# Kernel optimization log

Hardware: AMD Instinct MI355X
Metric: run time of the kernel (lower is better)

Reference implementation:

```python
import jax, jax.numpy as jnp
import numpy as np

D_MODEL = 1024
D_STATE = 64
D_CONV = 4
EXPAND = 2
HEADDIM = 128
NGROUPS = 1
D_INNER = EXPAND * D_MODEL                      # 2048
NHEADS = D_INNER // HEADDIM                     # 16
CONV_DIM = D_INNER + 2 * NGROUPS * D_STATE      # 2176
D_IN_PROJ = 2 * D_INNER + 2 * NGROUPS * D_STATE + NHEADS  # 4240
CHUNK = 64
B, L = 4, 2048


def segsum(x):
    # x: (..., l) -> (..., l, l); entry [i, j] = sum_{k=j+1..i} x_k (lower-tri, -inf above)
    l = x.shape[-1]
    cs = jnp.cumsum(x, -1)
    d = cs[..., :, None] - cs[..., None, :]
    mask = jnp.tril(jnp.ones((l, l), bool))
    return jnp.where(mask, d, -jnp.inf)


def setup_inputs() -> dict:
    key = jax.random.key(0)
    ks = jax.random.split(key, 8)
    x = jax.random.normal(ks[0], (B, L), jnp.float32)
    w_embed = jax.random.normal(ks[1], (D_MODEL,), jnp.float32)       # Linear(1, d_model) weight
    ln_g = jnp.ones((D_MODEL,), jnp.float32)
    ln_b = jnp.zeros((D_MODEL,), jnp.float32)
    W_in = jax.random.normal(ks[2], (D_IN_PROJ, D_MODEL), jnp.float32) * 0.02
    conv_w = jax.random.normal(ks[3], (CONV_DIM, D_CONV), jnp.float32) * 0.1
    conv_b = jnp.zeros((CONV_DIM,), jnp.float32)
    dt0 = jnp.exp(jax.random.uniform(ks[4], (NHEADS,), jnp.float32) * (np.log(0.1) - np.log(0.001)) + np.log(0.001))
    dt_bias = jnp.log(jnp.expm1(dt0))  # inverse softplus (mamba2 init)
    A_log = jnp.log(jax.random.uniform(ks[5], (NHEADS,), jnp.float32, minval=1.0, maxval=16.0))
    D = jnp.ones((NHEADS,), jnp.float32)
    rms_w = jnp.ones((D_INNER,), jnp.float32)
    W_out = jax.random.normal(ks[6], (D_MODEL, D_INNER), jnp.float32) * 0.02
    return {"x": x, "w_embed": w_embed, "ln_g": ln_g, "ln_b": ln_b, "W_in": W_in,
            "conv_w": conv_w, "conv_b": conv_b, "dt_bias": dt_bias, "A_log": A_log,
            "D": D, "rms_w": rms_w, "W_out": W_out}


def reference(x, w_embed, ln_g, ln_b, W_in, conv_w, conv_b, dt_bias, A_log, D, rms_w, W_out):
    # in_proj: Linear(1, d_model, bias=False)
    h = x[..., None] * w_embed                     # (B, L, d_model)
    # LayerNorm
    mu = jnp.mean(h, -1, keepdims=True)
    var = jnp.mean((h - mu) ** 2, -1, keepdims=True)
    h = (h - mu) * jax.lax.rsqrt(var + 1e-5) * ln_g + ln_b
    # ---- Mamba2 block ----
    zxbcdt = h @ W_in.T                            # (B, L, D_IN_PROJ)
    z, xBC, dt = jnp.split(zxbcdt, [D_INNER, D_INNER + CONV_DIM], axis=-1)
    dt = jax.nn.softplus(dt + dt_bias)             # (B, L, H)
    # causal depthwise conv1d + silu
    xp = jnp.pad(xBC, ((0, 0), (D_CONV - 1, 0), (0, 0)))
    conv = conv_b + sum(xp[:, k:k + L, :] * conv_w[:, k] for k in range(D_CONV))
    xBC = jax.nn.silu(conv)
    xs, Bm, Cm = jnp.split(xBC, [D_INNER, D_INNER + NGROUPS * D_STATE], axis=-1)
    X = xs.reshape(B, L, NHEADS, HEADDIM)
    rep = NHEADS // NGROUPS
    Bh = jnp.repeat(Bm.reshape(B, L, NGROUPS, D_STATE), rep, axis=2)   # (B,L,H,N)
    Ch = jnp.repeat(Cm.reshape(B, L, NGROUPS, D_STATE), rep, axis=2)
    A = -jnp.exp(A_log)                            # (H,)
    dA = dt * A                                    # (B, L, H)
    Xd = X * dt[..., None]                         # (B, L, H, P)
    # chunked SSD scan (math-equivalent to the selective-scan recurrence)
    nc = L // CHUNK
    Xc = Xd.reshape(B, nc, CHUNK, NHEADS, HEADDIM)
    Bc = Bh.reshape(B, nc, CHUNK, NHEADS, D_STATE)
    Cc = Ch.reshape(B, nc, CHUNK, NHEADS, D_STATE)
    Ac = dA.reshape(B, nc, CHUNK, NHEADS).transpose(0, 3, 1, 2)        # (B,H,c,l)
    Acs = jnp.cumsum(Ac, -1)
    Lmat = jnp.exp(segsum(Ac))                                          # (B,H,c,l,l)
    Y_diag = jnp.einsum('bclhn,bcshn,bhcls,bcshp->bclhp', Cc, Bc, Lmat, Xc)
    decay_states = jnp.exp(Acs[..., -1:] - Acs)
    states = jnp.einsum('bclhn,bhcl,bclhp->bchpn', Bc, decay_states, Xc)
    states = jnp.concatenate([jnp.zeros_like(states[:, :1]), states], axis=1)
    decay_chunk = jnp.exp(segsum(jnp.pad(Acs[..., -1], ((0, 0), (0, 0), (1, 0)))))
    prev_states = jnp.einsum('bhzc,bchpn->bzhpn', decay_chunk, states)[:, :-1]
    Y_off = jnp.einsum('bclhn,bchpn,bhcl->bclhp', Cc, prev_states, jnp.exp(Acs))
    Y = (Y_diag + Y_off).reshape(B, L, NHEADS, HEADDIM) + X * D[None, None, :, None]
    y = Y.reshape(B, L, D_INNER)
    # gated RMSNorm then out_proj
    y = y * jax.nn.silu(z)
    y = y * jax.lax.rsqrt(jnp.mean(y * y, -1, keepdims=True) + 1e-5) * rms_w
    return y @ W_out.T
```

## Files before the change

kernel.cpp:

```cpp
#include <hip/hip_runtime.h>

#define DEV __device__ __forceinline__

typedef __bf16 bf16x8 __attribute__((ext_vector_type(8)));
typedef float f32x4 __attribute__((ext_vector_type(4)));

#define BB 4
#define LL 2048
#define DMODEL 1024
#define DINNER 2048
#define NHEADS 16
#define HEADDIM 128
#define DSTATE 64
#define CONVDIM 2176
#define DINPROJ 4240
#define NCHUNK 32
#define ROWS (BB*LL)

#define OF_A    ((size_t)0)
#define OF_ST   ((size_t)32768)
#define OF_P    ((size_t)65536)
#define OF_Q    ((size_t)98304)
#define OF_WO   ((size_t)131072)
#define OF_CONV ((size_t)8388608)
#define OF_Y    ((size_t)50331648)
#define OF_YBF  ((size_t)100663296)
#define OF_SP   ((size_t)150994944)
#define OF_ACS  ((size_t)190840832)
#define OF_ECS  ((size_t)191365120)

DEV void gload_lds16(const void* g, void* l) {
  __builtin_amdgcn_global_load_lds((const __attribute__((address_space(1))) void*)g,
                                   (__attribute__((address_space(3))) void*)l, 16, 0, 0);
}

DEV char* swaddr(char* base, int r, int c) {
  return base + r * 128 + (((c) * 2) ^ (((r) & 7) << 4));
}

__global__ __launch_bounds__(256) void stats_kernel(
    const float* __restrict__ w, float* __restrict__ st)
{
  int t = threadIdx.x;
  float s = 0.f, s2 = 0.f;
  #pragma unroll
  for (int j = 0; j < 4; j++) { float v = w[t + 256 * j]; s += v; s2 += v * v; }
  #pragma unroll
  for (int m = 32; m; m >>= 1) { s += __shfl_xor(s, m); s2 += __shfl_xor(s2, m); }
  __shared__ float rs[4], rs2[4];
  if ((t & 63) == 0) { rs[t >> 6] = s; rs2[t >> 6] = s2; }
  __syncthreads();
  if (t == 0) {
    float S = rs[0] + rs[1] + rs[2] + rs[3];
    float S2 = rs2[0] + rs2[1] + rs2[2] + rs2[3];
    float mu = S * (1.f / DMODEL);
    st[0] = mu;
    st[1] = S2 * (1.f / DMODEL) - mu * mu;
  }
}

__global__ __launch_bounds__(256) void prep_a_kernel(
    const float* __restrict__ x, const float* __restrict__ st, float* __restrict__ a)
{
  int r = blockIdx.x * 256 + threadIdx.x;
  float varw = st[1];
  float xv = x[r];
  a[r] = xv * rsqrtf(xv * xv * varw + 1e-5f);
}

__global__ __launch_bounds__(256) void gemv_kernel(
    const float* __restrict__ w, const float* __restrict__ g,
    const float* __restrict__ beta, const float* __restrict__ st,
    const float* __restrict__ W, float* __restrict__ p, float* __restrict__ q)
{
  int t = threadIdx.x;
  int j = blockIdx.x * 16 + (t >> 4);
  int l16 = t & 15;
  float wbar = st[0];
  const float* Wr = W + (size_t)j * DMODEL;
  float ap = 0.f, aq = 0.f;
  #pragma unroll 4
  for (int jj = 0; jj < 64; jj++) {
    int i = jj * 16 + l16;
    float Wv = Wr[i];
    ap += (w[i] - wbar) * g[i] * Wv;
    aq += beta[i] * Wv;
  }
  #pragma unroll
  for (int m = 8; m; m >>= 1) { ap += __shfl_xor(ap, m, 16); aq += __shfl_xor(aq, m, 16); }
  if (l16 == 0) { p[j] = ap; q[j] = aq; }
}

__global__ __launch_bounds__(256) void convert_wo_kernel(
    const float* __restrict__ Wo, __bf16* __restrict__ Wob)
{
  const int NO = DMODEL * DINNER;
  for (int i = blockIdx.x * 256 + threadIdx.x; i < NO; i += gridDim.x * 256)
    Wob[i] = (__bf16)Wo[i];
}

__global__ __launch_bounds__(256) void conv2_kernel(
    const float* __restrict__ a, const float* __restrict__ p,
    const float* __restrict__ q, const float* __restrict__ conv_w,
    const float* __restrict__ conv_b, __bf16* __restrict__ out)
{
  int gidx = blockIdx.x * 256 + threadIdx.x;
  if (gidx >= ROWS * (CONVDIM / 8)) return;
  int cg = gidx % (CONVDIM / 8);
  int row = gidx / (CONVDIM / 8);
  int l = row & (LL - 1);
  int ch = cg * 8;
  float av[4];
  #pragma unroll
  for (int k = 0; k < 4; k++) {
    int li = l + k - 3;
    av[k] = (li >= 0) ? a[row + k - 3] : 0.f;
  }
  bf16x8 o;
  #pragma unroll
  for (int jj = 0; jj < 8; jj++) {
    int c = ch + jj;
    f32x4 cw = *(const f32x4*)(conv_w + c * 4);
    float px = p[DINNER + c], qx = q[DINNER + c];
    float sacw = 0.f, scw = 0.f;
    #pragma unroll
    for (int k = 0; k < 4; k++) {
      int li = l + k - 3;
      if (li >= 0) { sacw += av[k] * cw[k]; scw += cw[k]; }
    }
    float val = conv_b[c] + qx * scw + px * sacw;
    o[jj] = (__bf16)(val / (1.f + __expf(-val)));
  }
  *(bf16x8*)(out + (size_t)row * CONVDIM + ch) = o;
}

__global__ __launch_bounds__(256) void ssd_chunk_kernel(
    const __bf16* __restrict__ conv, const float* __restrict__ a,
    const float* __restrict__ p, const float* __restrict__ q,
    const float* __restrict__ dt_bias, const float* __restrict__ A_log,
    __bf16* __restrict__ Y, __bf16* __restrict__ S,
    float* __restrict__ acs, float* __restrict__ ecs)
{
  __shared__ __align__(16) char sm[49664];
  char* smC  = sm;
  char* smB  = sm + 8192;
  char* smBd = sm + 16384;
  char* smG  = sm + 24576;
  char* smX  = sm + 32768;
  float* sAcs = (float*)(sm + 49152);
  float* sDec = (float*)(sm + 49408);

  int bx = blockIdx.x;
  int c = bx & 31, h = (bx >> 5) & 15, b = bx >> 9;
  int t = threadIdx.x;
  int lane = t & 63, w = t >> 6;
  int row0 = b * LL + c * 64;
  const __bf16* cr = conv + (size_t)(row0 + lane) * CONVDIM;

  float av = a[row0 + lane];
  float vx = av * p[DINNER + CONVDIM + h] + q[DINNER + CONVDIM + h] + dt_bias[h];
  float dtv = vx > 15.f ? vx : log1pf(__expf(vx));

  bf16x8 bch[2], cch[2], xch[4];
  #pragma unroll
  for (int k = 0; k < 2; k++) {
    int c8 = w * 16 + 8 * k;
    bch[k] = *(const bf16x8*)(cr + DINNER + c8);
    cch[k] = *(const bf16x8*)(cr + DINNER + DSTATE + c8);
  }
  #pragma unroll
  for (int k = 0; k < 4; k++)
    xch[k] = *(const bf16x8*)(cr + h * HEADDIM + w * 8 + 32 * k);

  if (t < 64) {
    float Ah = -__expf(A_log[h]);
    float cs = dtv * Ah;
    #pragma unroll
    for (int off = 1; off < 64; off <<= 1) {
      float o = __shfl_up(cs, off);
      if (lane >= off) cs += o;
    }
    float cend = __shfl(cs, 63);
    sAcs[lane] = cs;
    sDec[lane] = __expf(cend - cs);
    acs[(((size_t)b * NHEADS + h) * NCHUNK + c) * 64 + lane] = cs;
    if (lane == 63) ecs[((size_t)b * NHEADS + h) * NCHUNK + c] = __expf(cend);
  }

  #pragma unroll
  for (int k = 0; k < 2; k++) {
    int c8 = w * 16 + 8 * k;
    *(bf16x8*)swaddr(smB, lane, c8) = bch[k];
    *(bf16x8*)swaddr(smC, lane, c8) = cch[k];
  }
  #pragma unroll
  for (int k = 0; k < 4; k++) {
    int p0 = w * 8 + 32 * k;
    #pragma unroll
    for (int j = 0; j < 8; j++)
      *(__bf16*)swaddr(smX, p0 + j, lane) = (__bf16)((float)xch[k][j] * dtv);
  }
  __syncthreads();

  float decv = sDec[lane];
  #pragma unroll
  for (int k = 0; k < 2; k++) {
    int c8 = w * 16 + 8 * k;
    #pragma unroll
    for (int j = 0; j < 8; j++)
      *(__bf16*)swaddr(smBd, c8 + j, lane) = (__bf16)((float)bch[k][j] * decv);
  }

  int lr = lane & 15, kb = (lane >> 4) * 8;
  int rl = 16 * w + (lane >> 4) * 4;

  {
    bf16x8 af[2];
    #pragma unroll
    for (int ks = 0; ks < 2; ks++)
      af[ks] = *(const bf16x8*)swaddr(smC, 16 * w + lr, ks * 32 + kb);
    f32x4 g[4] = {};
    #pragma unroll
    for (int nt = 0; nt < 4; nt++)
      #pragma unroll
      for (int ks = 0; ks < 2; ks++) {
        bf16x8 bm = *(const bf16x8*)swaddr(smB, 16 * nt + lr, ks * 32 + kb);
        g[nt] = __builtin_amdgcn_mfma_f32_16x16x32_bf16(af[ks], bm, g[nt], 0, 0, 0);
      }
    #pragma unroll
    for (int nt = 0; nt < 4; nt++)
      #pragma unroll
      for (int qq = 0; qq < 4; qq++) {
        int gl = rl + qq, gs = 16 * nt + lr;
        float val = (gl >= gs) ? g[nt][qq] * __expf(sAcs[gl] - sAcs[gs]) : 0.f;
        *(__bf16*)swaddr(smG, gl, gs) = (__bf16)val;
      }
  }
  __syncthreads();

  {
    bf16x8 af[2];
    #pragma unroll
    for (int ks = 0; ks < 2; ks++)
      af[ks] = *(const bf16x8*)swaddr(smG, 16 * w + lr, ks * 32 + kb);
    f32x4 y[8] = {};
    #pragma unroll
    for (int nt = 0; nt < 8; nt++)
      #pragma unroll
      for (int ks = 0; ks < 2; ks++) {
        bf16x8 bm = *(const bf16x8*)swaddr(smX, 16 * nt + lr, ks * 32 + kb);
        y[nt] = __builtin_amdgcn_mfma_f32_16x16x32_bf16(af[ks], bm, y[nt], 0, 0, 0);
      }
    #pragma unroll
    for (int nt = 0; nt < 8; nt++)
      #pragma unroll
      for (int qq = 0; qq < 4; qq++)
        Y[(size_t)(row0 + rl + qq) * DINNER + h * HEADDIM + 16 * nt + lr] = (__bf16)y[nt][qq];
  }

  {
    bf16x8 bfs[4][2];
    #pragma unroll
    for (int nt = 0; nt < 4; nt++)
      #pragma unroll
      for (int ks = 0; ks < 2; ks++)
        bfs[nt][ks] = *(const bf16x8*)swaddr(smBd, 16 * nt + lr, ks * 32 + kb);
    f32x4 s4[2][4] = {};
    #pragma unroll
    for (int mi = 0; mi < 2; mi++) {
      bf16x8 af[2];
      #pragma unroll
      for (int ks = 0; ks < 2; ks++)
        af[ks] = *(const bf16x8*)swaddr(smX, 32 * w + 16 * mi + lr, ks * 32 + kb);
      #pragma unroll
      for (int nt = 0; nt < 4; nt++)
        #pragma unroll
        for (int ks = 0; ks < 2; ks++)
          s4[mi][nt] = __builtin_amdgcn_mfma_f32_16x16x32_bf16(af[ks], bfs[nt][ks], s4[mi][nt], 0, 0, 0);
    }
    __bf16* Sp = S + (((size_t)b * NCHUNK + c) * NHEADS + h) * (HEADDIM * DSTATE);
    #pragma unroll
    for (int mi = 0; mi < 2; mi++)
      #pragma unroll
      for (int nt = 0; nt < 4; nt++)
        #pragma unroll
        for (int qq = 0; qq < 4; qq++) {
          int pp = 32 * w + 16 * mi + (lane >> 4) * 4 + qq;
          Sp[pp * DSTATE + 16 * nt + lr] = (__bf16)s4[mi][nt][qq];
        }
  }
}

__global__ __launch_bounds__(256) void scan_kernel(
    __bf16* SP, const float* __restrict__ ecs)
{
  int t = blockIdx.x * 256 + threadIdx.x;
  int n = t & 63, p = (t >> 6) & 127, h = (t >> 13) & 15, b = t >> 17;
  float P = 0.f;
  for (int c = 0; c < NCHUNK; c++) {
    size_t idx = (((size_t)b * NCHUNK + c) * NHEADS + h) * (HEADDIM * DSTATE) + (size_t)p * DSTATE + n;
    float s = (float)SP[idx];
    SP[idx] = (__bf16)P;
    float e = ecs[((size_t)b * NHEADS + h) * NCHUNK + c];
    P = e * P + s;
  }
}

__global__ __launch_bounds__(256) void ssd_off_kernel(
    const __bf16* __restrict__ conv, const __bf16* __restrict__ P,
    const float* __restrict__ acs, const float* __restrict__ Dp,
    __bf16* __restrict__ Y)
{
  __shared__ __align__(16) char sm[24832];
  char* smC = sm;
  char* smP = sm + 8192;
  float* eA = (float*)(sm + 24576);
  int bx = blockIdx.x;
  int c = bx & 31, h = (bx >> 5) & 15, b = bx >> 9;
  int t = threadIdx.x;
  int lane = t & 63, w = t >> 6;
  int row0 = b * LL + c * 64;
  #pragma unroll
  for (int k = 0; k < 2; k++) {
    int qg = t + 256 * k;
    int lq = qg >> 3, c8 = (qg & 7) * 8;
    bf16x8 v = *(const bf16x8*)(conv + (size_t)(row0 + lq) * CONVDIM + DINNER + DSTATE + c8);
    *(bf16x8*)swaddr(smC, lq, c8) = v;
  }
  const __bf16* Pp = P + (((size_t)b * NCHUNK + c) * NHEADS + h) * (HEADDIM * DSTATE);
  #pragma unroll
  for (int k = 0; k < 4; k++) {
    int qg = t + 256 * k;
    int pr = qg >> 3, c8 = (qg & 7) * 8;
    bf16x8 v = *(const bf16x8*)(Pp + pr * DSTATE + c8);
    *(bf16x8*)swaddr(smP, pr, c8) = v;
  }
  if (t < 64) eA[t] = __expf(acs[(((size_t)b * NHEADS + h) * NCHUNK + c) * 64 + t]);
  __syncthreads();
  int lr = lane & 15, kb = (lane >> 4) * 8;
  bf16x8 af[2];
  #pragma unroll
  for (int ks = 0; ks < 2; ks++)
    af[ks] = *(const bf16x8*)swaddr(smC, 16 * w + lr, ks * 32 + kb);
  f32x4 y[8] = {};
  #pragma unroll
  for (int nt = 0; nt < 8; nt++)
    #pragma unroll
    for (int ks = 0; ks < 2; ks++) {
      bf16x8 bm = *(const bf16x8*)swaddr(smP, 16 * nt + lr, ks * 32 + kb);
      y[nt] = __builtin_amdgcn_mfma_f32_16x16x32_bf16(af[ks], bm, y[nt], 0, 0, 0);
    }
  float Dh = Dp[h];
  int rl = 16 * w + (lane >> 4) * 4;
  #pragma unroll
  for (int nt = 0; nt < 8; nt++)
    #pragma unroll
    for (int qq = 0; qq < 4; qq++) {
      int l = rl + qq;
      int pp = 16 * nt + lr;
      size_t yi = (size_t)(row0 + l) * DINNER + h * HEADDIM + pp;
      float xsv = (float)conv[(size_t)(row0 + l) * CONVDIM + h * HEADDIM + pp];
      Y[yi] = (__bf16)((float)Y[yi] + eA[l] * y[nt][qq] + Dh * xsv);
    }
}

__global__ __launch_bounds__(256) void gate_norm_kernel(
    const __bf16* __restrict__ Y, const float* __restrict__ a,
    const float* __restrict__ p, const float* __restrict__ q,
    const float* __restrict__ rms_w, __bf16* __restrict__ ybf)
{
  int row = blockIdx.x, t = threadIdx.x;
  float ar = a[row];
  float v[8]; float ss = 0.f;
  #pragma unroll
  for (int j = 0; j < 8; j++) {
    int i = t + j * 256;
    float zv = ar * p[i] + q[i];
    float yv = (float)Y[(size_t)row * DINNER + i];
    float g = yv * (zv / (1.f + __expf(-zv)));
    v[j] = g; ss += g * g;
  }
  #pragma unroll
  for (int m = 32; m; m >>= 1) ss += __shfl_xor(ss, m);
  __shared__ float red[4];
  if ((t & 63) == 0) red[t >> 6] = ss;
  __syncthreads();
  float tot = red[0] + red[1] + red[2] + red[3];
  float r = rsqrtf(tot * (1.f / DINNER) + 1e-5f);
  #pragma unroll
  for (int j = 0; j < 8; j++) {
    int i = t + j * 256;
    ybf[(size_t)row * DINNER + i] = (__bf16)(v[j] * r * rms_w[i]);
  }
}

__global__ __launch_bounds__(512, 2) void gemm_op_kernel(
    const __bf16* __restrict__ A, const __bf16* __restrict__ Bt,
    float* __restrict__ C, int K, int N)
{
  extern __shared__ char sm[];
  const int t = threadIdx.x;
  const int lane = t & 63, w = t >> 6;
  const int wr = w >> 1, wc = w & 1;

  int nbn = gridDim.x;
  int nwg = nbn * gridDim.y;
  int lid = blockIdx.y * nbn + blockIdx.x;
  int wg = (lid & 7) * (nwg >> 3) + (lid >> 3);
  int m0 = (wg / nbn) * 256, n0 = (wg % nbn) * 128;

  int r0, c0, r1, c1;
  {
    int y0 = t * 16, pg0 = y0 >> 7;
    int in0 = (y0 & 127) ^ ((pg0 & 7) << 4);
    r0 = pg0 * 2 + (in0 >> 6); c0 = in0 & 63;
    int y1 = 8192 + t * 16, pg1 = y1 >> 7;
    int in1 = (y1 & 127) ^ ((pg1 & 7) << 4);
    r1 = pg1 * 2 + (in1 >> 6); c1 = in1 & 63;
  }
  const char* pA0 = (const char*)A + (size_t)(m0 + r0) * (2 * K) + c0;
  const char* pA1 = (const char*)A + (size_t)(m0 + r1) * (2 * K) + c1;
  const char* pB0 = (const char*)Bt + (size_t)(n0 + r0) * (2 * K) + c0;

  const int lr = lane & 15, kg = lane >> 4;
  int rA = wr * 64 + lr, pgA = rA >> 1;
  const int offA = pgA * 128 + ((((rA & 1) << 6) | (kg << 4)) ^ ((pgA & 7) << 4));
  int rB = wc * 64 + lr, pgB = rB >> 1;
  const int offB = pgB * 128 + ((((rB & 1) << 6) | (kg << 4)) ^ ((pgB & 7) << 4));

  f32x4 acc[4][4] = {};
  const int KT = K >> 5;

  #define STG(slot) do { \
    char* la_ = sm + (slot) * 16384; \
    char* lb_ = sm + 65536 + (slot) * 8192; \
    gload_lds16(pA0, la_ + t * 16); \
    gload_lds16(pA1, la_ + 8192 + t * 16); \
    gload_lds16(pB0, lb_ + t * 16); \
    pA0 += 64; pA1 += 64; pB0 += 64; \
  } while (0)

  STG(0); STG(1); STG(2);
  asm volatile("s_waitcnt vmcnt(6)" ::: "memory");
  __builtin_amdgcn_sched_barrier(0);
  __builtin_amdgcn_s_barrier();

  for (int kt = 0; kt < KT; ++kt) {
    int s = kt & 3;
    if (kt + 3 < KT) STG((kt + 3) & 3);
    const char* sa = sm + s * 16384;
    const char* sb = sm + 65536 + s * 8192;
    bf16x8 af[4], bfr[4];
    #pragma unroll
    for (int m = 0; m < 4; m++) af[m] = *(const bf16x8*)(sa + offA + m * 1024);
    #pragma unroll
    for (int n = 0; n < 4; n++) bfr[n] = *(const bf16x8*)(sb + offB + n * 1024);
    __builtin_amdgcn_s_setprio(1);
    #pragma unroll
    for (int m = 0; m < 4; m++)
      #pragma unroll
      for (int n = 0; n < 4; n++)
        acc[m][n] = __builtin_amdgcn_mfma_f32_16x16x32_bf16(af[m], bfr[n], acc[m][n], 0, 0, 0);
    __builtin_amdgcn_s_setprio(0);
    if (kt + 3 < KT)      { asm volatile("s_waitcnt vmcnt(6)" ::: "memory"); }
    else if (kt + 2 < KT) { asm volatile("s_waitcnt vmcnt(3)" ::: "memory"); }
    else if (kt + 1 < KT) { asm volatile("s_waitcnt vmcnt(0)" ::: "memory"); }
    __builtin_amdgcn_sched_barrier(0);
    __builtin_amdgcn_s_barrier();
  }
  #undef STG

  #pragma unroll
  for (int m = 0; m < 4; m++)
    #pragma unroll
    for (int n = 0; n < 4; n++)
      #pragma unroll
      for (int qq = 0; qq < 4; qq++) {
        int row = m0 + wr * 64 + m * 16 + kg * 4 + qq;
        int col = n0 + wc * 64 + n * 16 + lr;
        C[(size_t)row * N + col] = acc[m][n][qq];
      }
}

extern "C" void kernel_launch(void* const* d_in, const int* in_sizes, int n_in,
                              void* d_out, int out_size, void* d_ws, size_t ws_size,
                              hipStream_t stream) {
  const float* x       = (const float*)d_in[0];
  const float* w_embed = (const float*)d_in[1];
  const float* ln_g    = (const float*)d_in[2];
  const float* ln_b    = (const float*)d_in[3];
  const float* W_in    = (const float*)d_in[4];
  const float* conv_w  = (const float*)d_in[5];
  const float* conv_b  = (const float*)d_in[6];
  const float* dt_bias = (const float*)d_in[7];
  const float* A_log   = (const float*)d_in[8];
  const float* Dp      = (const float*)d_in[9];
  const float* rms_w   = (const float*)d_in[10];
  const float* W_out   = (const float*)d_in[11];
  char* ws = (char*)d_ws;
  float*  aR   = (float*)(ws + OF_A);
  float*  st   = (float*)(ws + OF_ST);
  float*  pV   = (float*)(ws + OF_P);
  float*  qV   = (float*)(ws + OF_Q);
  __bf16* Wob  = (__bf16*)(ws + OF_WO);
  __bf16* convb = (__bf16*)(ws + OF_CONV);
  __bf16* Ybf  = (__bf16*)(ws + OF_Y);
  __bf16* ybf  = (__bf16*)(ws + OF_YBF);
  __bf16* SP   = (__bf16*)(ws + OF_SP);
  float*  acs  = (float*)(ws + OF_ACS);
  float*  ecs  = (float*)(ws + OF_ECS);
  float*  out  = (float*)d_out;

  hipFuncSetAttribute((const void*)gemm_op_kernel,
                      hipFuncAttributeMaxDynamicSharedMemorySize, 98304);

  stats_kernel<<<1, 256, 0, stream>>>(w_embed, st);
  prep_a_kernel<<<ROWS / 256, 256, 0, stream>>>(x, st, aR);
  gemv_kernel<<<DINPROJ / 16, 256, 0, stream>>>(w_embed, ln_g, ln_b, st, W_in, pV, qV);
  convert_wo_kernel<<<1024, 256, 0, stream>>>(W_out, Wob);
  conv2_kernel<<<(ROWS * (CONVDIM / 8) + 255) / 256, 256, 0, stream>>>(
      aR, pV, qV, conv_w, conv_b, convb);
  ssd_chunk_kernel<<<BB * NHEADS * NCHUNK, 256, 0, stream>>>(
      convb, aR, pV, qV, dt_bias, A_log, Ybf, SP, acs, ecs);
  scan_kernel<<<(BB * NHEADS * HEADDIM * DSTATE) / 256, 256, 0, stream>>>(SP, ecs);
  ssd_off_kernel<<<BB * NHEADS * NCHUNK, 256, 0, stream>>>(convb, SP, acs, Dp, Ybf);
  gate_norm_kernel<<<ROWS, 256, 0, stream>>>(Ybf, aR, pV, qV, rms_w, ybf);
  gemm_op_kernel<<<dim3(8, 32), 512, 98304, stream>>>(ybf, Wob, out, DINNER, DMODEL);
}
```

Baseline: 279.6 us.

## Fuse depthwise conv+SiLU recomputation into SSD kernels, drop conv buffer

Removes the separate conv2 kernel and its bf16 conv output buffer (8192 rows × 2176 channels). The SSD chunk and off-diagonal kernels now recompute the rank-1 conv+SiLU values directly from the scalar input a, p and q. This trades a large global write and two reads for redundant per-block arithmetic and exp evaluations. B/C channels are recomputed in every head block, sixteen times per position.

```diff
diff --git a/kernel.cpp b/kernel.cpp
--- a/kernel.cpp
+++ b/kernel.cpp
@@ -22,7 +22,6 @@
 #define OF_P    ((size_t)65536)
 #define OF_Q    ((size_t)98304)
 #define OF_WO   ((size_t)131072)
-#define OF_CONV ((size_t)8388608)
 #define OF_Y    ((size_t)50331648)
 #define OF_YBF  ((size_t)100663296)
 #define OF_SP   ((size_t)150994944)
@@ -36,6 +35,16 @@
 
 DEV char* swaddr(char* base, int r, int c) {
   return base + r * 128 + (((c) * 2) ^ (((r) & 7) << 4));
+}
+
+DEV float convsilu(int ch, const float* __restrict__ conv_w, const float* __restrict__ conv_b,
+                   const float* __restrict__ p, const float* __restrict__ q,
+                   const float av[4], const float mk[4]) {
+  f32x4 w4 = *(const f32x4*)(conv_w + ch * 4);
+  float sa = av[0] * w4[0] + av[1] * w4[1] + av[2] * w4[2] + av[3] * w4[3];
+  float sm = mk[0] * w4[0] + mk[1] * w4[1] + mk[2] * w4[2] + mk[3] * w4[3];
+  float val = conv_b[ch] + q[DINNER + ch] * sm + p[DINNER + ch] * sa;
+  return val / (1.f + __expf(-val));
 }
 
 __global__ __launch_bounds__(256) void stats_kernel(
@@ -99,45 +108,11 @@
     Wob[i] = (__bf16)Wo[i];
 }
 
-__global__ __launch_bounds__(256) void conv2_kernel(
+__global__ __launch_bounds__(256) void ssd_chunk_kernel(
     const float* __restrict__ a, const float* __restrict__ p,
     const float* __restrict__ q, const float* __restrict__ conv_w,
-    const float* __restrict__ conv_b, __bf16* __restrict__ out)
-{
-  int gidx = blockIdx.x * 256 + threadIdx.x;
-  if (gidx >= ROWS * (CONVDIM / 8)) return;
-  int cg = gidx % (CONVDIM / 8);
-  int row = gidx / (CONVDIM / 8);
-  int l = row & (LL - 1);
-  int ch = cg * 8;
-  float av[4];
-  #pragma unroll
-  for (int k = 0; k < 4; k++) {
-    int li = l + k - 3;
-    av[k] = (li >= 0) ? a[row + k - 3] : 0.f;
-  }
-  bf16x8 o;
-  #pragma unroll
-  for (int jj = 0; jj < 8; jj++) {
-    int c = ch + jj;
-    f32x4 cw = *(const f32x4*)(conv_w + c * 4);
-    float px = p[DINNER + c], qx = q[DINNER + c];
-    float sacw = 0.f, scw = 0.f;
-    #pragma unroll
-    for (int k = 0; k < 4; k++) {
-      int li = l + k - 3;
-      if (li >= 0) { sacw += av[k] * cw[k]; scw += cw[k]; }
-    }
-    float val = conv_b[c] + qx * scw + px * sacw;
-    o[jj] = (__bf16)(val / (1.f + __expf(-val)));
-  }
-  *(bf16x8*)(out + (size_t)row * CONVDIM + ch) = o;
-}
-
-__global__ __launch_bounds__(256) void ssd_chunk_kernel(
-    const __bf16* __restrict__ conv, const float* __restrict__ a,
-    const float* __restrict__ p, const float* __restrict__ q,
-    const float* __restrict__ dt_bias, const float* __restrict__ A_log,
+    const float* __restrict__ conv_b, const float* __restrict__ dt_bias,
+    const float* __restrict__ A_log,
     __bf16* __restrict__ Y, __bf16* __restrict__ S,
     float* __restrict__ acs, float* __restrict__ ecs)
 {
@@ -155,22 +130,48 @@
   int t = threadIdx.x;
   int lane = t & 63, w = t >> 6;
   int row0 = b * LL + c * 64;
-  const __bf16* cr = conv + (size_t)(row0 + lane) * CONVDIM;
-
-  float av = a[row0 + lane];
-  float vx = av * p[DINNER + CONVDIM + h] + q[DINNER + CONVDIM + h] + dt_bias[h];
+
+  float av[4], mk[4];
+  {
+    int lg = c * 64 + lane;
+    #pragma unroll
+    for (int k = 0; k < 4; k++) {
+      int li = lg + k - 3;
+      bool v = li >= 0;
+      av[k] = v ? a[b * LL + li] : 0.f;
+      mk[k] = v ? 1.f : 0.f;
+    }
+  }
+
+  float vx = av[3] * p[DINNER + CONVDIM + h] + q[DINNER + CONVDIM + h] + dt_bias[h];
   float dtv = vx > 15.f ? vx : log1pf(__expf(vx));
 
-  bf16x8 bch[2], cch[2], xch[4];
+  float bv[16];
   #pragma unroll
   for (int k = 0; k < 2; k++) {
     int c8 = w * 16 + 8 * k;
-    bch[k] = *(const bf16x8*)(cr + DINNER + c8);
-    cch[k] = *(const bf16x8*)(cr + DINNER + DSTATE + c8);
-  }
-  #pragma unroll
-  for (int k = 0; k < 4; k++)
-    xch[k] = *(const bf16x8*)(cr + h * HEADDIM + w * 8 + 32 * k);
+    bf16x8 vb, vc;
+    #pragma unroll
+    for (int j = 0; j < 8; j++) {
+      int n = c8 + j;
+      float bb = convsilu(2048 + n, conv_w, conv_b, p, q, av, mk);
+      float cc = convsilu(2112 + n, conv_w, conv_b, p, q, av, mk);
+      bv[8 * k + j] = bb;
+      vb[j] = (__bf16)bb;
+      vc[j] = (__bf16)cc;
+    }
+    *(bf16x8*)swaddr(smB, lane, c8) = vb;
+    *(bf16x8*)swaddr(smC, lane, c8) = vc;
+  }
+  #pragma unroll
+  for (int k = 0; k < 4; k++) {
+    int p0 = w * 8 + 32 * k;
+    #pragma unroll
+    for (int j = 0; j < 8; j++) {
+      float xv2 = convsilu(h * HEADDIM + p0 + j, conv_w, conv_b, p, q, av, mk);
+      *(__bf16*)swaddr(smX, p0 + j, lane) = (__bf16)(xv2 * dtv);
+    }
+  }
 
   if (t < 64) {
     float Ah = -__expf(A_log[h]);
@@ -186,29 +187,15 @@
     acs[(((size_t)b * NHEADS + h) * NCHUNK + c) * 64 + lane] = cs;
     if (lane == 63) ecs[((size_t)b * NHEADS + h) * NCHUNK + c] = __expf(cend);
   }
-
+  __syncthreads();
+
+  float decv = sDec[lane];
   #pragma unroll
   for (int k = 0; k < 2; k++) {
     int c8 = w * 16 + 8 * k;
-    *(bf16x8*)swaddr(smB, lane, c8) = bch[k];
-    *(bf16x8*)swaddr(smC, lane, c8) = cch[k];
-  }
-  #pragma unroll
-  for (int k = 0; k < 4; k++) {
-    int p0 = w * 8 + 32 * k;
     #pragma unroll
     for (int j = 0; j < 8; j++)
-      *(__bf16*)swaddr(smX, p0 + j, lane) = (__bf16)((float)xch[k][j] * dtv);
-  }
-  __syncthreads();
-
-  float decv = sDec[lane];
-  #pragma unroll
-  for (int k = 0; k < 2; k++) {
-    int c8 = w * 16 + 8 * k;
-    #pragma unroll
-    for (int j = 0; j < 8; j++)
-      *(__bf16*)swaddr(smBd, c8 + j, lane) = (__bf16)((float)bch[k][j] * decv);
+      *(__bf16*)swaddr(smBd, c8 + j, lane) = (__bf16)(bv[8 * k + j] * decv);
   }
 
   int lr = lane & 15, kb = (lane >> 4) * 8;
@@ -307,25 +294,46 @@
 }
 
 __global__ __launch_bounds__(256) void ssd_off_kernel(
-    const __bf16* __restrict__ conv, const __bf16* __restrict__ P,
+    const float* __restrict__ a, const float* __restrict__ p,
+    const float* __restrict__ q, const float* __restrict__ conv_w,
+    const float* __restrict__ conv_b, const __bf16* __restrict__ P,
     const float* __restrict__ acs, const float* __restrict__ Dp,
     __bf16* __restrict__ Y)
 {
-  __shared__ __align__(16) char sm[24832];
+  __shared__ __align__(16) char sm[25408];
   char* smC = sm;
   char* smP = sm + 8192;
   float* eA = (float*)(sm + 24576);
+  float* sA = (float*)(sm + 24832);
   int bx = blockIdx.x;
   int c = bx & 31, h = (bx >> 5) & 15, b = bx >> 9;
   int t = threadIdx.x;
   int lane = t & 63, w = t >> 6;
   int row0 = b * LL + c * 64;
-  #pragma unroll
-  for (int k = 0; k < 2; k++) {
-    int qg = t + 256 * k;
-    int lq = qg >> 3, c8 = (qg & 7) * 8;
-    bf16x8 v = *(const bf16x8*)(conv + (size_t)(row0 + lq) * CONVDIM + DINNER + DSTATE + c8);
-    *(bf16x8*)swaddr(smC, lq, c8) = v;
+
+  {
+    float av[4], mk[4];
+    int lg = c * 64 + lane;
+    #pragma unroll
+    for (int k = 0; k < 4; k++) {
+      int li = lg + k - 3;
+      bool v = li >= 0;
+      av[k] = v ? a[b * LL + li] : 0.f;
+      mk[k] = v ? 1.f : 0.f;
+    }
+    #pragma unroll
+    for (int k = 0; k < 2; k++) {
+      int c8 = w * 16 + 8 * k;
+      bf16x8 vc;
+      #pragma unroll
+      for (int j = 0; j < 8; j++)
+        vc[j] = (__bf16)convsilu(2112 + c8 + j, conv_w, conv_b, p, q, av, mk);
+      *(bf16x8*)swaddr(smC, lane, c8) = vc;
+    }
+  }
+  if (t < 67) {
+    int li = c * 64 + t - 3;
+    sA[t] = (li >= 0) ? a[b * LL + li] : 0.f;
   }
   const __bf16* Pp = P + (((size_t)b * NCHUNK + c) * NHEADS + h) * (HEADDIM * DSTATE);
   #pragma unroll
@@ -337,6 +345,7 @@
   }
   if (t < 64) eA[t] = __expf(acs[(((size_t)b * NHEADS + h) * NCHUNK + c) * 64 + t]);
   __syncthreads();
+
   int lr = lane & 15, kb = (lane >> 4) * 8;
   bf16x8 af[2];
   #pragma unroll
@@ -353,15 +362,27 @@
   float Dh = Dp[h];
   int rl = 16 * w + (lane >> 4) * 4;
   #pragma unroll
-  for (int nt = 0; nt < 8; nt++)
+  for (int nt = 0; nt < 8; nt++) {
+    int ch = h * HEADDIM + 16 * nt + lr;
+    f32x4 w4 = *(const f32x4*)(conv_w + ch * 4);
+    float cb = conv_b[ch], px = p[DINNER + ch], qx = q[DINNER + ch];
     #pragma unroll
     for (int qq = 0; qq < 4; qq++) {
       int l = rl + qq;
-      int pp = 16 * nt + lr;
-      size_t yi = (size_t)(row0 + l) * DINNER + h * HEADDIM + pp;
-      float xsv = (float)conv[(size_t)(row0 + l) * CONVDIM + h * HEADDIM + pp];
+      float sa = sA[l] * w4[0] + sA[l + 1] * w4[1] + sA[l + 2] * w4[2] + sA[l + 3] * w4[3];
+      float smv;
+      if (c > 0) smv = w4[0] + w4[1] + w4[2] + w4[3];
+      else {
+        smv = w4[3];
+        #pragma unroll
+        for (int k = 0; k < 3; k++) if (l + k >= 3) smv += w4[k];
+      }
+      float val = cb + qx * smv + px * sa;
+      float xsv = val / (1.f + __expf(-val));
+      size_t yi = (size_t)(row0 + l) * DINNER + ch;
       Y[yi] = (__bf16)((float)Y[yi] + eA[l] * y[nt][qq] + Dh * xsv);
     }
+  }
 }
 
 __global__ __launch_bounds__(256) void gate_norm_kernel(
@@ -503,7 +524,6 @@
   float*  pV   = (float*)(ws + OF_P);
   float*  qV   = (float*)(ws + OF_Q);
   __bf16* Wob  = (__bf16*)(ws + OF_WO);
-  __bf16* convb = (__bf16*)(ws + OF_CONV);
   __bf16* Ybf  = (__bf16*)(ws + OF_Y);
   __bf16* ybf  = (__bf16*)(ws + OF_YBF);
   __bf16* SP   = (__bf16*)(ws + OF_SP);
@@ -518,12 +538,11 @@
   prep_a_kernel<<<ROWS / 256, 256, 0, stream>>>(x, st, aR);
   gemv_kernel<<<DINPROJ / 16, 256, 0, stream>>>(w_embed, ln_g, ln_b, st, W_in, pV, qV);
   convert_wo_kernel<<<1024, 256, 0, stream>>>(W_out, Wob);
-  conv2_kernel<<<(ROWS * (CONVDIM / 8) + 255) / 256, 256, 0, stream>>>(
-      aR, pV, qV, conv_w, conv_b, convb);
   ssd_chunk_kernel<<<BB * NHEADS * NCHUNK, 256, 0, stream>>>(
-      convb, aR, pV, qV, dt_bias, A_log, Ybf, SP, acs, ecs);
+      aR, pV, qV, conv_w, conv_b, dt_bias, A_log, Ybf, SP, acs, ecs);
   scan_kernel<<<(BB * NHEADS * HEADDIM * DSTATE) / 256, 256, 0, stream>>>(SP, ecs);
-  ssd_off_kernel<<<BB * NHEADS * NCHUNK, 256, 0, stream>>>(convb, SP, acs, Dp, Ybf);
+  ssd_off_kernel<<<BB * NHEADS * NCHUNK, 256, 0, stream>>>(
+      aR, pV, qV, conv_w, conv_b, SP, acs, Dp, Ybf);
   gate_norm_kernel<<<ROWS, 256, 0, stream>>>(Ybf, aR, pV, qV, rms_w, ybf);
   gemm_op_kernel<<<dim3(8, 32), 512, 98304, stream>>>(ybf, Wob, out, DINNER, DMODEL);
 }
```

Result: faster. 255.3 us (-8.7%).
